# Performance work log

Measured on AMD Instinct MI355X. Metric: run time of the kernel, lower is better.

Reference implementation:

```python
import jax, jax.numpy as jnp
import numpy as np

H = W = 1024
N_ITERS = 100  # fixed-iteration Jacobi color propagation (x = b + W x), approximates the direct sparse solve
OFFSETS = [(-1, -1), (-1, 0), (-1, 1), (0, -1), (0, 1), (1, -1), (1, 0), (1, 1)]


def rgb2yiq(rgb):
    rgb = rgb / 255.0
    y = rgb @ jnp.array([0.3, 0.59, 0.11], dtype=rgb.dtype)
    r = rgb[..., 0]
    b = rgb[..., 2]
    i = 0.74 * (r - y) - 0.27 * (b - y)
    q = 0.48 * (r - y) + 0.41 * (b - y)
    return jnp.stack([y, i, q], axis=-1)


def yiq2rgb(yiq):
    M = jnp.array([[1.0, 0.9468822170900693, 0.6235565819861433],
                   [1.0, -0.27478764629897834, -0.6356910791873801],
                   [1.0, -1.1085450346420322, 1.7090069284064666]], dtype=yiq.dtype)
    rgb = yiq @ M.T
    return jnp.clip(rgb, 0.0, 1.0) * 255.0


def _shift_stack(xpad, n, m):
    # xpad: padded-by-1 array; returns [8, n, m, ...] stack of the 8 non-center 3x3 neighbors
    return jnp.stack([xpad[1 + dx:1 + dx + n, 1 + dy:1 + dy + m] for dx, dy in OFFSETS], axis=0)


def colorize(gray_rgb, appendix_rgb):
    n, m = gray_rgb.shape[:2]
    isColored = jnp.abs(gray_rgb / 255.0 - appendix_rgb / 255.0).sum(axis=2) > 0.01  # [n,m] bool
    gray_yiq = rgb2yiq(gray_rgb)
    app_yiq = rgb2yiq(appendix_rgb)
    Y = gray_yiq[..., 0]              # luminance channel [n,m]
    IQ = app_yiq[..., 1:]             # chroma channels   [n,m,2]

    # --- per-pixel local-variance-weighted neighbor affinities (vectorized 3x3 gather) ---
    Ypad = jnp.pad(Y, 1)
    Vpad = jnp.pad(jnp.ones((n, m), Y.dtype), 1)
    nbr = _shift_stack(Ypad, n, m)    # [8,n,m] neighbor luminance (0 where out of bounds)
    valid = _shift_stack(Vpad, n, m)  # [8,n,m] in-bounds mask

    count = valid.sum(axis=0) + 1.0                              # neighbors + center
    mean = ((nbr * valid).sum(axis=0) + Y) / count
    var = (((nbr - mean) ** 2) * valid).sum(axis=0)
    var = (var + (Y - mean) ** 2) / count
    vs = jnp.maximum(0.6 * var, 2e-6)

    w = jnp.exp(-((nbr - Y) ** 2) / vs) * valid                  # [8,n,m]
    w = w / w.sum(axis=0)                                        # normalize over in-bounds neighbors
    w = w * (~isColored)[None, :, :]                             # colored rows are identity rows

    # --- solve (I - W) x = b  by Jacobi iteration  x <- b + W x ---
    b = jnp.where(isColored[..., None], IQ, 0.0)                 # [n,m,2]

    @jax.checkpoint
    def step(x, _):
        xp = jnp.pad(x, ((1, 1), (1, 1), (0, 0)))
        nb = _shift_stack(xp, n, m)                              # [8,n,m,2]
        x_new = b + jnp.einsum('knm,knmc->nmc', w, nb)
        return x_new, None

    x, _ = jax.lax.scan(step, b, None, length=N_ITERS)

    colorized = jnp.concatenate([Y[..., None], x], axis=-1)      # [n,m,3] YIQ
    return yiq2rgb(colorized)


def setup_inputs() -> dict:
    key = jax.random.key(0)
    k1, k2, k3 = jax.random.split(key, 3)
    gray = jax.random.uniform(k1, (H, W, 3), dtype=jnp.float32) * 255.0
    scribble = jax.random.uniform(k2, (H, W, 1)) < 0.05
    color = jax.random.uniform(k3, (H, W, 3), dtype=jnp.float32) * 255.0
    appendix = jnp.where(scribble, color, gray)
    return {"gray_rgb": gray, "appendix_rgb": appendix}


def reference(gray_rgb, appendix_rgb):
    return colorize(gray_rgb, appendix_rgb)
```

## Files before the change

### kernel.cpp

```cpp
#include <hip/hip_runtime.h>
#include <hip/hip_fp16.h>

#define Hh 1024
#define Ww 1024
#define PO 12
#define PS 1048
#define T 10
#define TILE 32
#define RG 52
#define XSH 54
#define NPX (RG * RG)

typedef unsigned int u32;

struct alignas(16) W8 { __half2 a, b, c, d; };

__device__ inline __half2 h2(u32 v) { return *(__half2*)&v; }
__device__ inline u32 u2(__half2 v) { return *(u32*)&v; }

__device__ inline void fma_lo(u32& acc, u32 w, u32 x) {
    asm("v_pk_fma_f16 %0, %1, %2, %0 op_sel_hi:[0,1,1]"
        : "+v"(acc) : "v"(w), "v"(x));
}
__device__ inline void fma_hi(u32& acc, u32 w, u32 x) {
    asm("v_pk_fma_f16 %0, %1, %2, %0 op_sel:[1,0,0] op_sel_hi:[1,1,1]"
        : "+v"(acc) : "v"(w), "v"(x));
}

typedef __attribute__((address_space(3))) u32 lds_u32_t;
typedef __attribute__((address_space(1))) const u32 glb_u32_t;

__global__ __launch_bounds__(256)
void prep_kernel(const float* __restrict__ gray, const float* __restrict__ app,
                 float* __restrict__ Ypad, u32* __restrict__ x0,
                 u32* __restrict__ x1, unsigned char* __restrict__ mask) {
    int px = blockIdx.x * 64 + threadIdx.x;
    int py = blockIdx.y * 4 + threadIdx.y;
    if (px >= PS || py >= PS) return;
    int p = py * PS + px;
    int i = py - PO, j = px - PO;
    float yv = 0.f;
    float2 bv = make_float2(0.f, 0.f);
    if (i >= 0 && i < Hh && j >= 0 && j < Ww) {
        int idx = i * Ww + j;
        const float s = 1.f / 255.f;
        float gr = gray[idx * 3 + 0] * s;
        float gg = gray[idx * 3 + 1] * s;
        float gb = gray[idx * 3 + 2] * s;
        float ar = app[idx * 3 + 0] * s;
        float ag = app[idx * 3 + 1] * s;
        float ab = app[idx * 3 + 2] * s;
        float diff = fabsf(gr - ar) + fabsf(gg - ag) + fabsf(gb - ab);
        bool colored = diff > 0.01f;
        yv = 0.3f * gr + 0.59f * gg + 0.11f * gb;
        float ay = 0.3f * ar + 0.59f * ag + 0.11f * ab;
        float ai = 0.74f * (ar - ay) - 0.27f * (ab - ay);
        float aq = 0.48f * (ar - ay) + 0.41f * (ab - ay);
        if (colored) bv = make_float2(ai, aq);
        mask[idx] = colored ? 1 : 0;
    }
    Ypad[p] = yv;
    __half2 h = __floats2half2_rn(bv.x, bv.y);
    x0[p] = u2(h);
    x1[p] = 0u;
}

__global__ __launch_bounds__(256)
void weights_kernel(const float* __restrict__ Ypad,
                    const unsigned char* __restrict__ mask,
                    W8* __restrict__ w) {
    int px = blockIdx.x * 64 + threadIdx.x;
    int py = blockIdx.y * 4 + threadIdx.y;
    if (px >= PS || py >= PS) return;
    int p = py * PS + px;
    int i = py - PO, j = px - PO;
    W8 out;
    out.a = __floats2half2_rn(0.f, 0.f);
    out.b = out.a; out.c = out.a; out.d = out.a;
    if (i >= 0 && i < Hh && j >= 0 && j < Ww) {
        float yc = Ypad[p];
        float yn[8];
        yn[0] = Ypad[p - PS - 1]; yn[1] = Ypad[p - PS]; yn[2] = Ypad[p - PS + 1];
        yn[3] = Ypad[p - 1];                            yn[4] = Ypad[p + 1];
        yn[5] = Ypad[p + PS - 1]; yn[6] = Ypad[p + PS]; yn[7] = Ypad[p + PS + 1];
        float vt = (i > 0) ? 1.f : 0.f;
        float vb = (i < Hh - 1) ? 1.f : 0.f;
        float vl = (j > 0) ? 1.f : 0.f;
        float vr = (j < Ww - 1) ? 1.f : 0.f;
        float v[8] = { vt * vl, vt, vt * vr, vl, vr, vb * vl, vb, vb * vr };

        float count = 1.f, s1 = yc;
#pragma unroll
        for (int k = 0; k < 8; ++k) { count += v[k]; s1 += v[k] * yn[k]; }
        float mean = s1 / count;
        float var = (yc - mean) * (yc - mean);
#pragma unroll
        for (int k = 0; k < 8; ++k) { float d = yn[k] - mean; var += v[k] * d * d; }
        var /= count;
        float vs = fmaxf(0.6f * var, 2e-6f);
        float inv_vs = 1.f / vs;

        float wk[8], ws = 0.f;
#pragma unroll
        for (int k = 0; k < 8; ++k) {
            float d = yn[k] - yc;
            wk[k] = v[k] * expf(-d * d * inv_vs);
            ws += wk[k];
        }
        if (mask[i * Ww + j]) {
            out.a = __floats2half2_rn(-0.0f, 0.f);
        } else {
            float scale = 1.f / ws;
            out.a = __floats2half2_rn(wk[0] * scale, wk[1] * scale);
            out.b = __floats2half2_rn(wk[2] * scale, wk[3] * scale);
            out.c = __floats2half2_rn(wk[4] * scale, wk[5] * scale);
            out.d = __floats2half2_rn(wk[6] * scale, wk[7] * scale);
        }
    }
    w[p] = out;
}

__global__ __launch_bounds__(256, 4)
void iter10p_kernel(const u32* __restrict__ xin, u32* __restrict__ xout,
                    const W8* __restrict__ w, const float* __restrict__ Ypad,
                    float* __restrict__ out, int writeRGB) {
    __shared__ __align__(16) u32 xsm[2][RG * XSH];
    int tid = threadIdx.x;

    int bid  = (int)blockIdx.y * 32 + (int)blockIdx.x;
    int nbid = (bid & 7) * 128 + (bid >> 3);
    int gi0 = (nbid >> 5) * TILE - T;
    int gj0 = (nbid & 31) * TILE - T;

    {
        int wv = tid >> 6;
        int ln = tid & 63;
        if (ln < RG) {
            const u32* gbase = xin + (size_t)(gi0 + wv * 13 + PO) * PS + (gj0 + PO) + ln;
#pragma unroll 1
            for (int k = 0; k < 13; ++k) {
                __builtin_amdgcn_global_load_lds((glb_u32_t*)(gbase + (size_t)k * PS),
                                                 (lds_u32_t*)&xsm[0][(wv * 13 + k) * XSH],
                                                 4, 0, 0);
            }
        }
    }

    bool active = tid < 250;
    int s  = tid / 25;
    int cp = tid - s * 25;
    int r0 = 1 + 5 * s;
    int c0 = 1 + 2 * cp;

    u32 wq[5][8];
    u32 kL[5], kR[5];
    if (active) {
#pragma unroll
        for (int i = 0; i < 5; ++i) {
            int gp = (gi0 + r0 + i + PO) * PS + (gj0 + c0 + PO);
            const uint4* wp = (const uint4*)(w + gp);
            uint4 wa = wp[0];
            uint4 wb = wp[1];
            wq[i][0] = wa.x; wq[i][1] = wa.y; wq[i][2] = wa.z; wq[i][3] = wa.w;
            wq[i][4] = wb.x; wq[i][5] = wb.y; wq[i][6] = wb.z; wq[i][7] = wb.w;
            kL[i] = (wa.x & 0x8000u) ? 0xFFFFFFFFu : 0u;
            kR[i] = (wb.x & 0x8000u) ? 0xFFFFFFFFu : 0u;
        }
    }
    __syncthreads();

    int cur = 0;
#pragma unroll 1
    for (int t = 0; t < T; ++t) {
        int nxt = cur ^ 1;
        if (active) {
            const uint2* rp;
            uint2 u0, u1, m0, m1;
            rp = (const uint2*)&xsm[cur][(r0 - 1) * XSH]; u0 = rp[cp]; u1 = rp[cp + 1];
            rp = (const uint2*)&xsm[cur][r0 * XSH];       m0 = rp[cp]; m1 = rp[cp + 1];
#pragma unroll
            for (int i = 0; i < 5; ++i) {
                uint2 d0, d1;
                rp = (const uint2*)&xsm[cur][(r0 + i + 1) * XSH];
                d0 = rp[cp]; d1 = rp[cp + 1];

                u32 accL = kL[i] & m0.y;
                fma_lo(accL, wq[i][0], u0.x);
                fma_hi(accL, wq[i][0], u0.y);
                fma_lo(accL, wq[i][1], u1.x);
                fma_hi(accL, wq[i][1], m0.x);
                fma_lo(accL, wq[i][2], m1.x);
                fma_hi(accL, wq[i][2], d0.x);
                fma_lo(accL, wq[i][3], d0.y);
                fma_hi(accL, wq[i][3], d1.x);

                u32 accR = kR[i] & m1.x;
                fma_lo(accR, wq[i][4], u0.y);
                fma_hi(accR, wq[i][4], u1.x);
                fma_lo(accR, wq[i][5], u1.y);
                fma_hi(accR, wq[i][5], m0.y);
                fma_lo(accR, wq[i][6], m1.y);
                fma_hi(accR, wq[i][6], d0.y);
                fma_lo(accR, wq[i][7], d1.x);
                fma_hi(accR, wq[i][7], d1.y);

                int wp2 = (r0 + i) * XSH + c0;
                xsm[nxt][wp2]     = accL;
                xsm[nxt][wp2 + 1] = accR;

                u0 = m0; u1 = m1; m0 = d0; m1 = d1;
            }
        }
        __syncthreads();
        cur = nxt;
    }

    if (!writeRGB) {
#pragma unroll
        for (int k = 0; k < 4; ++k) {
            int pidx = tid + k * 256;
            int r = T + (pidx >> 5), c = T + (pidx & 31);
            xout[(gi0 + r + PO) * PS + (gj0 + c + PO)] = xsm[cur][r * XSH + c];
        }
    } else {
#pragma unroll
        for (int k = 0; k < 4; ++k) {
            int pidx = tid + k * 256;
            int r = T + (pidx >> 5), c = T + (pidx & 31);
            int gi = gi0 + r, gj = gj0 + c;
            float y = Ypad[(gi + PO) * PS + (gj + PO)];
            u32 pxv = xsm[cur][r * XSH + c];
            float2 iq = __half22float2(h2(pxv));
            float R_ = y + 0.9468822170900693f * iq.x + 0.6235565819861433f * iq.y;
            float G_ = y - 0.27478764629897834f * iq.x - 0.6356910791873801f * iq.y;
            float B_ = y - 1.1085450346420322f * iq.x + 1.7090069284064666f * iq.y;
            int idx = gi * Ww + gj;
            out[idx * 3 + 0] = fminf(fmaxf(R_, 0.f), 1.f) * 255.f;
            out[idx * 3 + 1] = fminf(fmaxf(G_, 0.f), 1.f) * 255.f;
            out[idx * 3 + 2] = fminf(fmaxf(B_, 0.f), 1.f) * 255.f;
        }
    }
}

extern "C" void kernel_launch(void* const* d_in, const int* in_sizes, int n_in,
                              void* d_out, int out_size, void* d_ws, size_t ws_size,
                              hipStream_t stream) {
    const float* gray = (const float*)d_in[0];
    const float* app  = (const float*)d_in[1];
    float* out = (float*)d_out;

    char* ws = (char*)d_ws;
    size_t off = 0;
    auto alloc = [&](size_t bytes) -> void* {
        void* r = ws + off;
        off = (off + bytes + 255) & ~(size_t)255;
        return r;
    };
    float* Ypad = (float*)alloc((size_t)PS * PS * sizeof(float));
    W8*    w    = (W8*)   alloc((size_t)PS * PS * sizeof(W8));
    unsigned char* mask = (unsigned char*)alloc((size_t)Hh * Ww);
    u32*   x0   = (u32*)  alloc((size_t)PS * PS * sizeof(u32));
    u32*   x1   = (u32*)  alloc((size_t)PS * PS * sizeof(u32));

    dim3 blk(64, 4);
    dim3 gridPad((PS + 63) / 64, (PS + 3) / 4);
    prep_kernel<<<gridPad, blk, 0, stream>>>(gray, app, Ypad, x0, x1, mask);
    weights_kernel<<<gridPad, blk, 0, stream>>>(Ypad, mask, w);

    dim3 gridIter(Ww / TILE, Hh / TILE);
    u32* xin = x0;
    u32* xout = x1;
    for (int l = 0; l < 10; ++l) {
        int last = (l == 9) ? 1 : 0;
        iter10p_kernel<<<gridIter, 256, 0, stream>>>(xin, xout, w, Ypad, out, last);
        u32* tmp = xin; xin = xout; xout = tmp;
    }
}
```

Baseline: 234.1 us.

## Split chroma field into even/odd column planes to avoid LDS bank conflicts

Stores the half2 chroma field as separate even-column and odd-column planes, both in global memory and in shared memory, in place of one interleaved row. Each thread's two-pixel column pair now reads consecutive 32-bit words from each plane instead of 64-bit strided uint2 loads, which is meant to remove LDS bank conflicts and make stores unit-stride. The cost is more load instructions per stencil row and scattered parity-dependent writes to global memory in prep and writeback.

```diff
diff --git a/kernel.cpp b/kernel.cpp
--- a/kernel.cpp
+++ b/kernel.cpp
@@ -5,11 +5,12 @@
 #define Ww 1024
 #define PO 12
 #define PS 1048
+#define PH 524
 #define T 10
 #define TILE 32
 #define RG 52
-#define XSH 54
-#define NPX (RG * RG)
+#define HS 27
+#define PL (RG * HS)
 
 typedef unsigned int u32;
 
@@ -32,12 +33,13 @@
 
 __global__ __launch_bounds__(256)
 void prep_kernel(const float* __restrict__ gray, const float* __restrict__ app,
-                 float* __restrict__ Ypad, u32* __restrict__ x0,
-                 u32* __restrict__ x1, unsigned char* __restrict__ mask) {
+                 float* __restrict__ Ypad,
+                 u32* __restrict__ xE0, u32* __restrict__ xO0,
+                 u32* __restrict__ xE1, u32* __restrict__ xO1,
+                 unsigned char* __restrict__ mask) {
     int px = blockIdx.x * 64 + threadIdx.x;
     int py = blockIdx.y * 4 + threadIdx.y;
     if (px >= PS || py >= PS) return;
-    int p = py * PS + px;
     int i = py - PO, j = px - PO;
     float yv = 0.f;
     float2 bv = make_float2(0.f, 0.f);
@@ -59,10 +61,11 @@
         if (colored) bv = make_float2(ai, aq);
         mask[idx] = colored ? 1 : 0;
     }
-    Ypad[p] = yv;
-    __half2 h = __floats2half2_rn(bv.x, bv.y);
-    x0[p] = u2(h);
-    x1[p] = 0u;
+    Ypad[py * PS + px] = yv;
+    u32 hval = u2(__floats2half2_rn(bv.x, bv.y));
+    int p = py * PH + (px >> 1);
+    if (px & 1) { xO0[p] = hval; xO1[p] = 0u; }
+    else        { xE0[p] = hval; xE1[p] = 0u; }
 }
 
 __global__ __launch_bounds__(256)
@@ -121,10 +124,11 @@
 }
 
 __global__ __launch_bounds__(256, 4)
-void iter10p_kernel(const u32* __restrict__ xin, u32* __restrict__ xout,
+void iter10p_kernel(const u32* __restrict__ xE_in, const u32* __restrict__ xO_in,
+                    u32* __restrict__ xE_out, u32* __restrict__ xO_out,
                     const W8* __restrict__ w, const float* __restrict__ Ypad,
                     float* __restrict__ out, int writeRGB) {
-    __shared__ __align__(16) u32 xsm[2][RG * XSH];
+    __shared__ __align__(16) u32 xs[2][2][PL];
     int tid = threadIdx.x;
 
     int bid  = (int)blockIdx.y * 32 + (int)blockIdx.x;
@@ -135,12 +139,17 @@
     {
         int wv = tid >> 6;
         int ln = tid & 63;
-        if (ln < RG) {
-            const u32* gbase = xin + (size_t)(gi0 + wv * 13 + PO) * PS + (gj0 + PO) + ln;
+        if (ln < 26) {
+            int ch = (gj0 + PO) >> 1;
+            const u32* gE = xE_in + (size_t)(gi0 + wv * 13 + PO) * PH + ch + ln;
+            const u32* gO = xO_in + (size_t)(gi0 + wv * 13 + PO) * PH + ch + ln;
 #pragma unroll 1
             for (int k = 0; k < 13; ++k) {
-                __builtin_amdgcn_global_load_lds((glb_u32_t*)(gbase + (size_t)k * PS),
-                                                 (lds_u32_t*)&xsm[0][(wv * 13 + k) * XSH],
+                __builtin_amdgcn_global_load_lds((glb_u32_t*)(gE + (size_t)k * PH),
+                                                 (lds_u32_t*)&xs[0][0][(wv * 13 + k) * HS],
+                                                 4, 0, 0);
+                __builtin_amdgcn_global_load_lds((glb_u32_t*)(gO + (size_t)k * PH),
+                                                 (lds_u32_t*)&xs[0][1][(wv * 13 + k) * HS],
                                                  4, 0, 0);
             }
         }
@@ -174,41 +183,45 @@
     for (int t = 0; t < T; ++t) {
         int nxt = cur ^ 1;
         if (active) {
-            const uint2* rp;
-            uint2 u0, u1, m0, m1;
-            rp = (const uint2*)&xsm[cur][(r0 - 1) * XSH]; u0 = rp[cp]; u1 = rp[cp + 1];
-            rp = (const uint2*)&xsm[cur][r0 * XSH];       m0 = rp[cp]; m1 = rp[cp + 1];
+            const u32* xe = xs[cur][0];
+            const u32* xo = xs[cur][1];
+            u32* xen = xs[nxt][0];
+            u32* xon = xs[nxt][1];
+            int rb = (r0 - 1) * HS + cp;
+            u32 u0x = xe[rb], u0y = xo[rb], u1x = xe[rb + 1], u1y = xo[rb + 1];
+            rb += HS;
+            u32 m0x = xe[rb], m0y = xo[rb], m1x = xe[rb + 1], m1y = xo[rb + 1];
 #pragma unroll
             for (int i = 0; i < 5; ++i) {
-                uint2 d0, d1;
-                rp = (const uint2*)&xsm[cur][(r0 + i + 1) * XSH];
-                d0 = rp[cp]; d1 = rp[cp + 1];
-
-                u32 accL = kL[i] & m0.y;
-                fma_lo(accL, wq[i][0], u0.x);
-                fma_hi(accL, wq[i][0], u0.y);
-                fma_lo(accL, wq[i][1], u1.x);
-                fma_hi(accL, wq[i][1], m0.x);
-                fma_lo(accL, wq[i][2], m1.x);
-                fma_hi(accL, wq[i][2], d0.x);
-                fma_lo(accL, wq[i][3], d0.y);
-                fma_hi(accL, wq[i][3], d1.x);
-
-                u32 accR = kR[i] & m1.x;
-                fma_lo(accR, wq[i][4], u0.y);
-                fma_hi(accR, wq[i][4], u1.x);
-                fma_lo(accR, wq[i][5], u1.y);
-                fma_hi(accR, wq[i][5], m0.y);
-                fma_lo(accR, wq[i][6], m1.y);
-                fma_hi(accR, wq[i][6], d0.y);
-                fma_lo(accR, wq[i][7], d1.x);
-                fma_hi(accR, wq[i][7], d1.y);
-
-                int wp2 = (r0 + i) * XSH + c0;
-                xsm[nxt][wp2]     = accL;
-                xsm[nxt][wp2 + 1] = accR;
-
-                u0 = m0; u1 = m1; m0 = d0; m1 = d1;
+                int rd = (r0 + i + 1) * HS + cp;
+                u32 d0x = xe[rd], d0y = xo[rd], d1x = xe[rd + 1], d1y = xo[rd + 1];
+
+                u32 accL = kL[i] & m0y;
+                fma_lo(accL, wq[i][0], u0x);
+                fma_hi(accL, wq[i][0], u0y);
+                fma_lo(accL, wq[i][1], u1x);
+                fma_hi(accL, wq[i][1], m0x);
+                fma_lo(accL, wq[i][2], m1x);
+                fma_hi(accL, wq[i][2], d0x);
+                fma_lo(accL, wq[i][3], d0y);
+                fma_hi(accL, wq[i][3], d1x);
+
+                u32 accR = kR[i] & m1x;
+                fma_lo(accR, wq[i][4], u0y);
+                fma_hi(accR, wq[i][4], u1x);
+                fma_lo(accR, wq[i][5], u1y);
+                fma_hi(accR, wq[i][5], m0y);
+                fma_lo(accR, wq[i][6], m1y);
+                fma_hi(accR, wq[i][6], d0y);
+                fma_lo(accR, wq[i][7], d1x);
+                fma_hi(accR, wq[i][7], d1y);
+
+                int wb = (r0 + i) * HS + cp;
+                xon[wb]     = accL;
+                xen[wb + 1] = accR;
+
+                u0x = m0x; u0y = m0y; u1x = m1x; u1y = m1y;
+                m0x = d0x; m0y = d0y; m1x = d1x; m1y = d1y;
             }
         }
         __syncthreads();
@@ -220,7 +233,9 @@
         for (int k = 0; k < 4; ++k) {
             int pidx = tid + k * 256;
             int r = T + (pidx >> 5), c = T + (pidx & 31);
-            xout[(gi0 + r + PO) * PS + (gj0 + c + PO)] = xsm[cur][r * XSH + c];
+            u32 val = xs[cur][c & 1][r * HS + (c >> 1)];
+            u32* pl = (c & 1) ? xO_out : xE_out;
+            pl[(size_t)(gi0 + r + PO) * PH + ((gj0 + PO + c) >> 1)] = val;
         }
     } else {
 #pragma unroll
@@ -229,7 +244,7 @@
             int r = T + (pidx >> 5), c = T + (pidx & 31);
             int gi = gi0 + r, gj = gj0 + c;
             float y = Ypad[(gi + PO) * PS + (gj + PO)];
-            u32 pxv = xsm[cur][r * XSH + c];
+            u32 pxv = xs[cur][c & 1][r * HS + (c >> 1)];
             float2 iq = __half22float2(h2(pxv));
             float R_ = y + 0.9468822170900693f * iq.x + 0.6235565819861433f * iq.y;
             float G_ = y - 0.27478764629897834f * iq.x - 0.6356910791873801f * iq.y;
@@ -259,20 +274,22 @@
     float* Ypad = (float*)alloc((size_t)PS * PS * sizeof(float));
     W8*    w    = (W8*)   alloc((size_t)PS * PS * sizeof(W8));
     unsigned char* mask = (unsigned char*)alloc((size_t)Hh * Ww);
-    u32*   x0   = (u32*)  alloc((size_t)PS * PS * sizeof(u32));
-    u32*   x1   = (u32*)  alloc((size_t)PS * PS * sizeof(u32));
+    u32*   xE0  = (u32*)  alloc((size_t)PS * PH * sizeof(u32));
+    u32*   xO0  = (u32*)  alloc((size_t)PS * PH * sizeof(u32));
+    u32*   xE1  = (u32*)  alloc((size_t)PS * PH * sizeof(u32));
+    u32*   xO1  = (u32*)  alloc((size_t)PS * PH * sizeof(u32));
 
     dim3 blk(64, 4);
     dim3 gridPad((PS + 63) / 64, (PS + 3) / 4);
-    prep_kernel<<<gridPad, blk, 0, stream>>>(gray, app, Ypad, x0, x1, mask);
+    prep_kernel<<<gridPad, blk, 0, stream>>>(gray, app, Ypad, xE0, xO0, xE1, xO1, mask);
     weights_kernel<<<gridPad, blk, 0, stream>>>(Ypad, mask, w);
 
     dim3 gridIter(Ww / TILE, Hh / TILE);
-    u32* xin = x0;
-    u32* xout = x1;
+    u32 *iE = xE0, *iO = xO0, *oE = xE1, *oO = xO1;
     for (int l = 0; l < 10; ++l) {
         int last = (l == 9) ? 1 : 0;
-        iter10p_kernel<<<gridIter, 256, 0, stream>>>(xin, xout, w, Ypad, out, last);
-        u32* tmp = xin; xin = xout; xout = tmp;
-    }
-}
+        iter10p_kernel<<<gridIter, 256, 0, stream>>>(iE, iO, oE, oO, w, Ypad, out, last);
+        u32* t0 = iE; iE = oE; oE = t0;
+        u32* t1 = iO; iO = oO; oO = t1;
+    }
+}
```

After: 244.3 us. +4.4%, slower.
